# Kernel tuning notes

Measured on AMD Instinct MI355X. Metric: run time of the kernel, lower is better.

Reference implementation:

```python
import jax, jax.numpy as jnp
import numpy as np
from jax import lax

VOCAB, E, H, B, T, NCLS = 50000, 1024, 1024, 1024, 64, 2

def setup_inputs() -> dict:
    key = jax.random.key(0)
    ks = jax.random.split(key, 10)
    s = 0.05
    return {
        "x": jax.random.randint(ks[0], (B, T), 0, VOCAB),
        "emb": jax.random.normal(ks[1], (VOCAB, E), jnp.float32) * s,
        "W_ih": jax.random.normal(ks[2], (4 * H, E), jnp.float32) * s,
        "W_hh": jax.random.normal(ks[3], (4 * H, H), jnp.float32) * s,
        "b_ih": jax.random.normal(ks[4], (4 * H,), jnp.float32) * s,
        "b_hh": jax.random.normal(ks[5], (4 * H,), jnp.float32) * s,
        "W_out": jax.random.normal(ks[6], (NCLS, H), jnp.float32) * s,
        "b_out": jax.random.normal(ks[7], (NCLS,), jnp.float32) * s,
        "h0": jax.random.normal(ks[8], (B, H), jnp.float32),
        "c0": jax.random.normal(ks[9], (B, H), jnp.float32),
    }

def reference(x, emb, W_ih, W_hh, b_ih, b_hh, W_out, b_out, h0, c0):
    # Embedding lookup then transpose to time-major, like x.transpose(1, 0)
    xe = emb[x]                      # [B, T, E]
    xt = jnp.swapaxes(xe, 0, 1)      # [T, B, E]

    def step(carry, xi):
        h, c = carry
        # nn.LSTMCell: gates in (i, f, g, o) order
        gates = xi @ W_ih.T + b_ih + h @ W_hh.T + b_hh  # [B, 4H]
        i, f, g, o = jnp.split(gates, 4, axis=-1)
        c2 = jax.nn.sigmoid(f) * c + jax.nn.sigmoid(i) * jnp.tanh(g)
        h2 = jax.nn.sigmoid(o) * jnp.tanh(c2)
        # Per-step classifier on cell state c (as in the original loop)
        logp = jax.nn.log_softmax(c2 @ W_out.T + b_out, axis=-1)
        return (h2, c2), logp

    (hT, cT), actions_pair = lax.scan(step, (h0, c0), xt)  # actions_pair: [T, B, NCLS]
    out_final = cT @ W_out.T + b_out                       # linear on last cell state
    return actions_pair, out_final
```

## Files before the change

kernel.cpp:

```cpp
#include <hip/hip_runtime.h>

typedef __bf16 bf16x8 __attribute__((ext_vector_type(8)));
typedef float f32x4 __attribute__((ext_vector_type(4)));
typedef unsigned short u16;
typedef unsigned int u32;

#define T_ 64
#define B_ 1024
#define H_ 1024
#define G4_ 4096
#define HB_ (B_ * H_)
#define NBLK_ 512
#define PARTSZ_ (B_ * 2 * 64)

__device__ inline u16 f2bf(float f) {
  u32 u = __float_as_uint(f);
  u32 r = (u + 0x7fffu + ((u >> 16) & 1u)) >> 16;
  return (u16)r;
}

__device__ inline uint2 cvt4(float4 v) {
  uint2 r;
  r.x = (u32)f2bf(v.x) | ((u32)f2bf(v.y) << 16);
  r.y = (u32)f2bf(v.z) | ((u32)f2bf(v.w) << 16);
  return r;
}

__device__ __forceinline__ void gload16(const void* g, void* l) {
  __builtin_amdgcn_global_load_lds(
      (const __attribute__((address_space(1))) unsigned int*)g,
      (__attribute__((address_space(3))) unsigned int*)l, 16, 0, 0);
}

__device__ __forceinline__ void gload16_nt(const void* g, void* l) {
  __builtin_amdgcn_global_load_lds(
      (const __attribute__((address_space(1))) unsigned int*)g,
      (__attribute__((address_space(3))) unsigned int*)l, 16, 0, 2);
}

__device__ __forceinline__ void store_wt16(u16* p, u16 v) {
  asm volatile("global_store_short %0, %1, off sc0 sc1" :: "v"(p), "v"((u32)v) : "memory");
}

__device__ inline float fsig(float x) { return 1.f / (1.f + __expf(-x)); }
__device__ inline float ftanh(float x) {
  float e = __expf(2.f * x);
  return 1.f - 2.f / (e + 1.f);
}

__global__ void prep_kernel(const float* __restrict__ W_ih, const float* __restrict__ W_hh,
                            const float* __restrict__ b_ih, const float* __restrict__ b_hh,
                            const float* __restrict__ h0,
                            u16* __restrict__ WihP, u16* __restrict__ WhhP,
                            float* __restrict__ bcP, u16* __restrict__ h0slot,
                            u32* __restrict__ flags) {
  int bid = blockIdx.x, tid = threadIdx.x;
  if (bid < 4096) {
    int np = bid;
    int gate = (np >> 4) & 3;
    int j = ((np >> 6) << 4) | (np & 15);
    size_t srow = (size_t)(gate * 1024 + j) * 1024;
    int base = tid << 2;
    *(uint2*)(WihP + (size_t)np * 1024 + base) = cvt4(*(const float4*)(W_ih + srow + base));
    *(uint2*)(WhhP + (size_t)np * 1024 + base) = cvt4(*(const float4*)(W_hh + srow + base));
  } else if (bid < 5120) {
    int i = ((bid - 4096) * 256 + tid) << 2;
    *(uint2*)(h0slot + i) = cvt4(*(const float4*)(h0 + i));
  } else if (bid == 5120) {
#pragma unroll
    for (int q = 0; q < 16; ++q) {
      int np = q * 256 + tid;
      int gate = (np >> 4) & 3;
      int j = ((np >> 6) << 4) | (np & 15);
      int srcn = gate * 1024 + j;
      bcP[np] = b_ih[srcn] + b_hh[srcn];
    }
  } else {
    int idx = ((bid - 5121) * 256 + tid) << 2;
    *(uint4*)(flags + idx) = uint4{0u, 0u, 0u, 0u};
  }
}

__global__ void gather_kernel(const int* __restrict__ x, const float* __restrict__ emb,
                              u16* __restrict__ XEall) {
  int b = blockIdx.x, tc = blockIdx.y;
  int row = x[b * T_ + tc];
  int e = threadIdx.x << 2;
  float4 v = *(const float4*)(emb + (size_t)row * H_ + e);
  *(uint2*)(XEall + ((size_t)tc * B_ + b) * H_ + e) = cvt4(v);
}

__global__ void __launch_bounds__(512, 4) xproj_kernel(
    const u16* __restrict__ XEc, const u16* __restrict__ WihP,
    const float* __restrict__ bcP, u16* __restrict__ GXc) {
  __shared__ char smem[49152];
  const int tid = threadIdx.x;
  const int lane = tid & 63;
  const int wave = tid >> 6;
  const int wm = wave >> 1;
  const int wn = wave & 1;
  const int hbid = blockIdx.x;
  const int xcd = hbid & 7;
  const int s10 = hbid >> 3;
  const int mg = s10 >> 6;
  const int rem = s10 & 63;
  const int n0 = (rem >> 1) * 128;
  const int m0 = (xcd * 32 + mg * 2 + (rem & 1)) * 256;

  const u16* srcA[4];
  const u16* srcB[2];
  int betaA[4], betaB[2];
#pragma unroll
  for (int s = 0; s < 4; ++s) {
    int beta = (s * 512 + tid) * 16;
    int row = beta >> 7;
    int colu = (beta & 127) ^ ((row & 7) << 4);
    srcA[s] = XEc + (size_t)(m0 + row) * 1024 + (colu >> 1);
    betaA[s] = beta;
  }
#pragma unroll
  for (int s = 0; s < 2; ++s) {
    int beta = (s * 512 + tid) * 16;
    int row = beta >> 7;
    int colu = (beta & 127) ^ ((row & 7) << 4);
    srcB[s] = WihP + (size_t)(n0 + row) * 1024 + (colu >> 1);
    betaB[s] = 32768 + beta;
  }

  f32x4 acc[4][4] = {};
  const int rsel = lane & 15;
  const int ksel = (lane >> 4) << 4;

  for (int kt = 0; kt < 16; ++kt) {
#pragma unroll
    for (int s = 0; s < 4; ++s) gload16(srcA[s], smem + betaA[s]);
#pragma unroll
    for (int s = 0; s < 2; ++s) gload16(srcB[s], smem + betaB[s]);
#pragma unroll
    for (int s = 0; s < 4; ++s) srcA[s] += 64;
#pragma unroll
    for (int s = 0; s < 2; ++s) srcB[s] += 64;
    __syncthreads();
#pragma unroll
    for (int kk = 0; kk < 2; ++kk) {
      const int colb = kk * 64 + ksel;
      bf16x8 af[4], bfr[4];
#pragma unroll
      for (int mi = 0; mi < 4; ++mi) {
        int row = wm * 64 + mi * 16 + rsel;
        af[mi] = *(const bf16x8*)(smem + row * 128 + (colb ^ ((row & 7) << 4)));
      }
#pragma unroll
      for (int ni = 0; ni < 4; ++ni) {
        int row = wn * 64 + ni * 16 + rsel;
        bfr[ni] = *(const bf16x8*)(smem + 32768 + row * 128 + (colb ^ ((row & 7) << 4)));
      }
#pragma unroll
      for (int mi = 0; mi < 4; ++mi)
#pragma unroll
        for (int ni = 0; ni < 4; ++ni)
          acc[mi][ni] = __builtin_amdgcn_mfma_f32_16x16x32_bf16(af[mi], bfr[ni], acc[mi][ni], 0, 0, 0);
    }
    __syncthreads();
  }

  const int rbase = (lane >> 4) << 2;
  const int cbase = lane & 15;
  float bc[4];
#pragma unroll
  for (int ni = 0; ni < 4; ++ni) bc[ni] = bcP[n0 + wn * 64 + ni * 16 + cbase];
#pragma unroll
  for (int mi = 0; mi < 4; ++mi) {
#pragma unroll
    for (int ni = 0; ni < 4; ++ni) {
      int gc = n0 + wn * 64 + ni * 16 + cbase;
#pragma unroll
      for (int r = 0; r < 4; ++r) {
        int gm = m0 + wm * 64 + mi * 16 + rbase + r;
        GXc[(size_t)gm * G4_ + gc] = f2bf(acc[mi][ni][r] + bc[ni]);
      }
    }
  }
}

__global__ void __launch_bounds__(512, 4) rec_kernel(
    const u16* __restrict__ h0slot, u16* __restrict__ hring,
    const u16* __restrict__ WhhP, const u16* __restrict__ GXall,
    const float* __restrict__ c0, float* __restrict__ partAll,
    const float* __restrict__ Wout, u32* __restrict__ flags) {
  __shared__ char smem[81920];
  const int tid = threadIdx.x;
  const int lane = tid & 63;
  const int qm = tid >> 6;
  const int hbid = blockIdx.x;
  const int L = (hbid & 7) * 64 + (hbid >> 3);
  const int bx = L >> 3;
  const int by = L & 7;
  const int n0 = bx * 64;
  const int m0 = by * 128;

  int offA[2], offGX[2], betaS[2];
  int offB, betaB;
#pragma unroll
  for (int s = 0; s < 2; ++s) {
    int beta = (s * 512 + tid) * 16;
    int row = beta >> 7;
    int colu = (beta & 127) ^ ((row & 7) << 4);
    offA[s] = (m0 + row) * 1024 + (colu >> 1);
    offGX[s] = (m0 + row) * G4_ + n0 + (colu >> 1);
    betaS[s] = beta;
  }
  {
    int beta = tid * 16;
    int row = beta >> 7;
    int colu = (beta & 127) ^ ((row & 7) << 4);
    offB = (n0 + row) * 1024 + (colu >> 1);
    betaB = beta;
  }

  const int rsel = lane & 15;
  const int ksel = (lane >> 4) << 4;
  const int rbase = (lane >> 4) << 2;
  const int cbase = lane & 15;
  const int j = bx * 16 + cbase;
  const float w0 = Wout[j], w1 = Wout[1024 + j];

  float creg[4];
#pragma unroll
  for (int r = 0; r < 4; ++r)
    creg[r] = c0[(size_t)(m0 + qm * 16 + rbase + r) * H_ + j];

#pragma unroll
  for (int s = 0; s < 2; ++s) gload16_nt(GXall + offGX[s], smem + 49152 + betaS[s]);

#pragma unroll 1
  for (int t = 0; t < T_; ++t) {
    gload16(WhhP + offB, smem + 32768 + betaB);

    if (t) {
      if (tid < 64) {
        const u32* fg = flags + (size_t)(t - 1) * NBLK_ + by * 64;
        int guard = 0;
        while (true) {
          u32 v = __hip_atomic_load(fg + tid, __ATOMIC_RELAXED, __HIP_MEMORY_SCOPE_AGENT);
          if (__all(v != 0)) break;
          __builtin_amdgcn_s_sleep(4);
          if (++guard > (1 << 18)) break;
        }
      }
      __syncthreads();
    }

    const u16* hbR = t ? (hring + (size_t)(t - 1) * HB_) : h0slot;
    u16* hbW = hring + (size_t)t * HB_;

#pragma unroll
    for (int s = 0; s < 2; ++s) gload16(hbR + offA[s], smem + betaS[s]);

    f32x4 acc[4] = {};
#pragma unroll
    for (int kt = 0; kt < 16; ++kt) {
      const int cur = kt & 1;
      const int abase = cur * 16384;
      const int bbase = 32768 + cur * 8192;
      if (kt < 15) {
        const int nab = (cur ^ 1) * 16384;
        const int nbb = 32768 + (cur ^ 1) * 8192;
        const int kadv = (kt + 1) * 64;
#pragma unroll
        for (int s = 0; s < 2; ++s) gload16(hbR + offA[s] + kadv, smem + nab + betaS[s]);
        gload16(WhhP + offB + kadv, smem + nbb + betaB);
        asm volatile("s_waitcnt vmcnt(3)" ::: "memory");
      } else {
        asm volatile("s_waitcnt vmcnt(0)" ::: "memory");
      }
      __builtin_amdgcn_s_barrier();
      __builtin_amdgcn_sched_barrier(0);
#pragma unroll
      for (int kk = 0; kk < 2; ++kk) {
        const int colb = kk * 64 + ksel;
        bf16x8 af, bfr[4];
        {
          int row = qm * 16 + rsel;
          af = *(const bf16x8*)(smem + abase + row * 128 + (colb ^ ((row & 7) << 4)));
        }
#pragma unroll
        for (int ni = 0; ni < 4; ++ni) {
          int row = ni * 16 + rsel;
          bfr[ni] = *(const bf16x8*)(smem + bbase + row * 128 + (colb ^ ((row & 7) << 4)));
        }
#pragma unroll
        for (int ni = 0; ni < 4; ++ni)
          acc[ni] = __builtin_amdgcn_mfma_f32_16x16x32_bf16(af, bfr[ni], acc[ni], 0, 0, 0);
      }
      __builtin_amdgcn_s_barrier();
      __builtin_amdgcn_sched_barrier(0);
    }

    const char* lsGX = smem + 49152 + (t & 1) * 16384;
#pragma unroll
    for (int r = 0; r < 4; ++r) {
      int grow = qm * 16 + rbase + r;
      int b = m0 + grow;
      int gxswz = (grow & 7) << 4;
      float gx0 = __uint_as_float(
          (u32)*(const u16*)(lsGX + ((grow << 7) | ((cbase << 1) ^ gxswz))) << 16);
      float gx1 = __uint_as_float(
          (u32)*(const u16*)(lsGX + ((grow << 7) | ((((16 + cbase) << 1)) ^ gxswz))) << 16);
      float gx2 = __uint_as_float(
          (u32)*(const u16*)(lsGX + ((grow << 7) | ((((32 + cbase) << 1)) ^ gxswz))) << 16);
      float gx3 = __uint_as_float(
          (u32)*(const u16*)(lsGX + ((grow << 7) | ((((48 + cbase) << 1)) ^ gxswz))) << 16);
      float gi = acc[0][r] + gx0;
      float gf = acc[1][r] + gx1;
      float gg = acc[2][r] + gx2;
      float go = acc[3][r] + gx3;
      float c2 = fsig(gf) * creg[r] + fsig(gi) * ftanh(gg);
      float h2 = fsig(go) * ftanh(c2);
      creg[r] = c2;
      store_wt16(hbW + (size_t)b * H_ + j, f2bf(h2));
    }

    if (t + 1 < T_) {
      const u16* GXn = GXall + (size_t)(t + 1) * B_ * G4_;
      const int gxb = 49152 + ((t + 1) & 1) * 16384;
#pragma unroll
      for (int s = 0; s < 2; ++s) gload16_nt(GXn + offGX[s], smem + gxb + betaS[s]);
      asm volatile("s_waitcnt vmcnt(2)" ::: "memory");
    } else {
      asm volatile("s_waitcnt vmcnt(0)" ::: "memory");
    }
    __syncthreads();
    if (tid == 0)
      __hip_atomic_store(flags + (size_t)t * NBLK_ + by * 64 + bx, 1u,
                         __ATOMIC_RELAXED, __HIP_MEMORY_SCOPE_AGENT);

    float* partW = partAll + (size_t)t * PARTSZ_;
#pragma unroll
    for (int r = 0; r < 4; ++r) {
      int b = m0 + qm * 16 + rbase + r;
      float p0 = creg[r] * w0, p1 = creg[r] * w1;
#pragma unroll
      for (int off = 1; off < 16; off <<= 1) {
        p0 += __shfl_xor(p0, off);
        p1 += __shfl_xor(p1, off);
      }
      if (cbase == 0) {
        partW[(b << 7) + bx] = p0;
        partW[(b << 7) + 64 + bx] = p1;
      }
    }
  }
}

__global__ void final_kernel(const float* __restrict__ partAll, const float* __restrict__ bout,
                             float* __restrict__ out) {
  int gid = blockIdx.x * 256 + threadIdx.x;
  int t = gid >> 11;
  int r = gid & 2047;
  int b = r >> 1, cls = r & 1;
  const float4* pp = (const float4*)(partAll + (size_t)t * PARTSZ_ + (b << 7) + cls * 64);
  float4 sv = {0.f, 0.f, 0.f, 0.f};
#pragma unroll
  for (int q = 0; q < 16; ++q) {
    float4 v = pp[q];
    sv.x += v.x; sv.y += v.y; sv.z += v.z; sv.w += v.w;
  }
  float l = sv.x + sv.y + sv.z + sv.w + bout[cls];
  float other = __shfl_xor(l, 1);
  float m = fmaxf(l, other);
  float ls = m + __logf(__expf(l - m) + __expf(other - m));
  out[(size_t)t * (B_ * 2) + b * 2 + cls] = l - ls;
  if (t == 63) out[(size_t)T_ * (B_ * 2) + b * 2 + cls] = l;
}

extern "C" void kernel_launch(void* const* d_in, const int* in_sizes, int n_in,
                              void* d_out, int out_size, void* d_ws, size_t ws_size,
                              hipStream_t stream) {
  const int* x      = (const int*)d_in[0];
  const float* emb  = (const float*)d_in[1];
  const float* W_ih = (const float*)d_in[2];
  const float* W_hh = (const float*)d_in[3];
  const float* b_ih = (const float*)d_in[4];
  const float* b_hh = (const float*)d_in[5];
  const float* W_out = (const float*)d_in[6];
  const float* b_out = (const float*)d_in[7];
  const float* h0   = (const float*)d_in[8];
  const float* c0   = (const float*)d_in[9];
  float* out = (float*)d_out;

  char* w = (char*)d_ws;
  u16* WihP = (u16*)w;   w += (size_t)G4_ * H_ * 2;
  u16* WhhP = (u16*)w;   w += (size_t)G4_ * H_ * 2;
  u16* XEall = (u16*)w;  w += (size_t)T_ * HB_ * 2;
  u16* GXall = (u16*)w;  w += (size_t)T_ * B_ * G4_ * 2;
  u16* h0slot = (u16*)w; w += (size_t)HB_ * 2;
  float* bcP = (float*)w;     w += (size_t)G4_ * 4;
  float* partAll = (float*)w; w += (size_t)T_ * PARTSZ_ * 4;
  u32* flags = (u32*)w;       w += (size_t)T_ * NBLK_ * 4;

  prep_kernel<<<5153, 256, 0, stream>>>(W_ih, W_hh, b_ih, b_hh, h0,
                                        WihP, WhhP, bcP, h0slot, flags);
  gather_kernel<<<dim3(B_, T_), 256, 0, stream>>>(x, emb, XEall);
  xproj_kernel<<<8192, 512, 0, stream>>>(XEall, WihP, bcP, GXall);
  rec_kernel<<<NBLK_, 512, 0, stream>>>(h0slot, XEall , WhhP, GXall, c0,
                                        partAll, W_out, flags);
  final_kernel<<<512, 256, 0, stream>>>(partAll, b_out, out);
}
```

Before: 1.606 ms.

## Enlarge recurrent kernel tile to 128x128 with 256 persistent blocks

The recurrent kernel now runs 256 blocks of 256 threads, each owning a 128x128 gate tile instead of 512 blocks with 128x64 tiles. Every wave computes a 4x4 grid of MFMA fragments, which gives more register-level reuse of the A and B fragments and halves the number of blocks polling flags per step. The next step's GX prefetch moves into the last k-iteration so it overlaps with compute. In exchange the kernel uses more LDS and registers per block and has fewer waves to hide latency on each serial timestep.

```diff
diff --git a/kernel.cpp b/kernel.cpp
--- a/kernel.cpp
+++ b/kernel.cpp
@@ -10,7 +10,7 @@
 #define H_ 1024
 #define G4_ 4096
 #define HB_ (B_ * H_)
-#define NBLK_ 512
+#define NBLK_ 256
 #define PARTSZ_ (B_ * 2 * 64)
 
 __device__ inline u16 f2bf(float f) {
@@ -183,70 +183,77 @@
   }
 }
 
-__global__ void __launch_bounds__(512, 4) rec_kernel(
+__global__ void __launch_bounds__(256, 1) rec_kernel(
     const u16* __restrict__ h0slot, u16* __restrict__ hring,
     const u16* __restrict__ WhhP, const u16* __restrict__ GXall,
     const float* __restrict__ c0, float* __restrict__ partAll,
     const float* __restrict__ Wout, u32* __restrict__ flags) {
-  __shared__ char smem[81920];
+  __shared__ char smem[131072];
   const int tid = threadIdx.x;
   const int lane = tid & 63;
-  const int qm = tid >> 6;
+  const int wave = tid >> 6;
+  const int qm = wave >> 1;
+  const int qn = wave & 1;
   const int hbid = blockIdx.x;
-  const int L = (hbid & 7) * 64 + (hbid >> 3);
+  const int L = (hbid & 7) * 32 + (hbid >> 3);
   const int bx = L >> 3;
   const int by = L & 7;
-  const int n0 = bx * 64;
+  const int n0 = bx * 128;
   const int m0 = by * 128;
 
-  int offA[2], offGX[2], betaS[2];
-  int offB, betaB;
-#pragma unroll
-  for (int s = 0; s < 2; ++s) {
-    int beta = (s * 512 + tid) * 16;
+  int offA[4], offB[4], betaS[4];
+  int offGX[8], betaG[8];
+#pragma unroll
+  for (int s = 0; s < 4; ++s) {
+    int beta = (s * 256 + tid) * 16;
     int row = beta >> 7;
     int colu = (beta & 127) ^ ((row & 7) << 4);
     offA[s] = (m0 + row) * 1024 + (colu >> 1);
+    offB[s] = (n0 + row) * 1024 + (colu >> 1);
+    betaS[s] = beta;
+  }
+#pragma unroll
+  for (int s = 0; s < 8; ++s) {
+    int beta = (s * 256 + tid) * 16;
+    int row = beta >> 8;
+    int colu = (beta & 255) ^ ((row & 7) << 4);
     offGX[s] = (m0 + row) * G4_ + n0 + (colu >> 1);
-    betaS[s] = beta;
-  }
-  {
-    int beta = tid * 16;
-    int row = beta >> 7;
-    int colu = (beta & 127) ^ ((row & 7) << 4);
-    offB = (n0 + row) * 1024 + (colu >> 1);
-    betaB = beta;
+    betaG[s] = beta;
   }
 
   const int rsel = lane & 15;
   const int ksel = (lane >> 4) << 4;
   const int rbase = (lane >> 4) << 2;
   const int cbase = lane & 15;
-  const int j = bx * 16 + cbase;
+  const int j = bx * 32 + qn * 16 + cbase;
   const float w0 = Wout[j], w1 = Wout[1024 + j];
 
-  float creg[4];
-#pragma unroll
-  for (int r = 0; r < 4; ++r)
-    creg[r] = c0[(size_t)(m0 + qm * 16 + rbase + r) * H_ + j];
-
-#pragma unroll
-  for (int s = 0; s < 2; ++s) gload16_nt(GXall + offGX[s], smem + 49152 + betaS[s]);
+  float creg[4][4];
+#pragma unroll
+  for (int mi = 0; mi < 4; ++mi)
+#pragma unroll
+    for (int r = 0; r < 4; ++r)
+      creg[mi][r] = c0[(size_t)(m0 + qm * 64 + mi * 16 + rbase + r) * H_ + j];
+
+#pragma unroll
+  for (int s = 0; s < 8; ++s) gload16_nt(GXall + offGX[s], smem + 65536 + betaG[s]);
 
 #pragma unroll 1
   for (int t = 0; t < T_; ++t) {
-    gload16(WhhP + offB, smem + 32768 + betaB);
+#pragma unroll
+    for (int s = 0; s < 4; ++s) gload16(WhhP + offB[s], smem + 32768 + betaS[s]);
 
     if (t) {
-      if (tid < 64) {
-        const u32* fg = flags + (size_t)(t - 1) * NBLK_ + by * 64;
+      if (tid < 32) {
+        const u32* fg = flags + (size_t)(t - 1) * NBLK_ + by * 32;
         int guard = 0;
         while (true) {
           u32 v = __hip_atomic_load(fg + tid, __ATOMIC_RELAXED, __HIP_MEMORY_SCOPE_AGENT);
-          if (__all(v != 0)) break;
+          if (__all(tid >= 32 || v != 0)) break;
           __builtin_amdgcn_s_sleep(4);
           if (++guard > (1 << 18)) break;
         }
+      } else {
       }
       __syncthreads();
     }
@@ -255,99 +262,114 @@
     u16* hbW = hring + (size_t)t * HB_;
 
 #pragma unroll
-    for (int s = 0; s < 2; ++s) gload16(hbR + offA[s], smem + betaS[s]);
-
-    f32x4 acc[4] = {};
+    for (int s = 0; s < 4; ++s) gload16(hbR + offA[s], smem + betaS[s]);
+
+    f32x4 acc[4][4] = {};
 #pragma unroll
     for (int kt = 0; kt < 16; ++kt) {
       const int cur = kt & 1;
       const int abase = cur * 16384;
-      const int bbase = 32768 + cur * 8192;
+      const int bbase = 32768 + cur * 16384;
       if (kt < 15) {
         const int nab = (cur ^ 1) * 16384;
-        const int nbb = 32768 + (cur ^ 1) * 8192;
+        const int nbb = 32768 + (cur ^ 1) * 16384;
         const int kadv = (kt + 1) * 64;
 #pragma unroll
-        for (int s = 0; s < 2; ++s) gload16(hbR + offA[s] + kadv, smem + nab + betaS[s]);
-        gload16(WhhP + offB + kadv, smem + nbb + betaB);
-        asm volatile("s_waitcnt vmcnt(3)" ::: "memory");
+        for (int s = 0; s < 4; ++s) gload16(hbR + offA[s] + kadv, smem + nab + betaS[s]);
+#pragma unroll
+        for (int s = 0; s < 4; ++s) gload16(WhhP + offB[s] + kadv, smem + nbb + betaS[s]);
+        asm volatile("s_waitcnt vmcnt(8)" ::: "memory");
       } else {
-        asm volatile("s_waitcnt vmcnt(0)" ::: "memory");
+        if (t + 1 < T_) {
+          const u16* GXn = GXall + (size_t)(t + 1) * B_ * G4_;
+          const int gxb = 65536 + ((t + 1) & 1) * 32768;
+#pragma unroll
+          for (int s = 0; s < 8; ++s) gload16_nt(GXn + offGX[s], smem + gxb + betaG[s]);
+          asm volatile("s_waitcnt vmcnt(8)" ::: "memory");
+        } else {
+          asm volatile("s_waitcnt vmcnt(0)" ::: "memory");
+        }
       }
       __builtin_amdgcn_s_barrier();
       __builtin_amdgcn_sched_barrier(0);
 #pragma unroll
       for (int kk = 0; kk < 2; ++kk) {
         const int colb = kk * 64 + ksel;
-        bf16x8 af, bfr[4];
-        {
-          int row = qm * 16 + rsel;
-          af = *(const bf16x8*)(smem + abase + row * 128 + (colb ^ ((row & 7) << 4)));
+        bf16x8 af[4], bfr[4];
+#pragma unroll
+        for (int mi = 0; mi < 4; ++mi) {
+          int row = qm * 64 + mi * 16 + rsel;
+          af[mi] = *(const bf16x8*)(smem + abase + row * 128 + (colb ^ ((row & 7) << 4)));
         }
 #pragma unroll
         for (int ni = 0; ni < 4; ++ni) {
-          int row = ni * 16 + rsel;
+          int row = qn * 64 + ni * 16 + rsel;
           bfr[ni] = *(const bf16x8*)(smem + bbase + row * 128 + (colb ^ ((row & 7) << 4)));
         }
 #pragma unroll
-        for (int ni = 0; ni < 4; ++ni)
-          acc[ni] = __builtin_amdgcn_mfma_f32_16x16x32_bf16(af, bfr[ni], acc[ni], 0, 0, 0);
+        for (int mi = 0; mi < 4; ++mi)
+#pragma unroll
+          for (int ni = 0; ni < 4; ++ni)
+            acc[mi][ni] = __builtin_amdgcn_mfma_f32_16x16x32_bf16(af[mi], bfr[ni], acc[mi][ni], 0, 0, 0);
       }
       __builtin_amdgcn_s_barrier();
       __builtin_amdgcn_sched_barrier(0);
     }
 
-    const char* lsGX = smem + 49152 + (t & 1) * 16384;
-#pragma unroll
-    for (int r = 0; r < 4; ++r) {
-      int grow = qm * 16 + rbase + r;
-      int b = m0 + grow;
-      int gxswz = (grow & 7) << 4;
-      float gx0 = __uint_as_float(
-          (u32)*(const u16*)(lsGX + ((grow << 7) | ((cbase << 1) ^ gxswz))) << 16);
-      float gx1 = __uint_as_float(
-          (u32)*(const u16*)(lsGX + ((grow << 7) | ((((16 + cbase) << 1)) ^ gxswz))) << 16);
-      float gx2 = __uint_as_float(
-          (u32)*(const u16*)(lsGX + ((grow << 7) | ((((32 + cbase) << 1)) ^ gxswz))) << 16);
-      float gx3 = __uint_as_float(
-          (u32)*(const u16*)(lsGX + ((grow << 7) | ((((48 + cbase) << 1)) ^ gxswz))) << 16);
-      float gi = acc[0][r] + gx0;
-      float gf = acc[1][r] + gx1;
-      float gg = acc[2][r] + gx2;
-      float go = acc[3][r] + gx3;
-      float c2 = fsig(gf) * creg[r] + fsig(gi) * ftanh(gg);
-      float h2 = fsig(go) * ftanh(c2);
-      creg[r] = c2;
-      store_wt16(hbW + (size_t)b * H_ + j, f2bf(h2));
+    const char* lsGX = smem + 65536 + (t & 1) * 32768;
+#pragma unroll
+    for (int mi = 0; mi < 4; ++mi) {
+#pragma unroll
+      for (int r = 0; r < 4; ++r) {
+        int grow = qm * 64 + mi * 16 + rbase + r;
+        int b = m0 + grow;
+        int gxswz = (grow & 7) << 4;
+        const char* gxrow = lsGX + (grow << 8);
+        float gx0 = __uint_as_float(
+            (u32)*(const u16*)(gxrow + ((((qn * 64 + cbase) << 1)) ^ gxswz)) << 16);
+        float gx1 = __uint_as_float(
+            (u32)*(const u16*)(gxrow + ((((qn * 64 + 16 + cbase) << 1)) ^ gxswz)) << 16);
+        float gx2 = __uint_as_float(
+            (u32)*(const u16*)(gxrow + ((((qn * 64 + 32 + cbase) << 1)) ^ gxswz)) << 16);
+        float gx3 = __uint_as_float(
+            (u32)*(const u16*)(gxrow + ((((qn * 64 + 48 + cbase) << 1)) ^ gxswz)) << 16);
+        float gi = acc[mi][0][r] + gx0;
+        float gf = acc[mi][1][r] + gx1;
+        float gg = acc[mi][2][r] + gx2;
+        float go = acc[mi][3][r] + gx3;
+        float c2 = fsig(gf) * creg[mi][r] + fsig(gi) * ftanh(gg);
+        float h2 = fsig(go) * ftanh(c2);
+        creg[mi][r] = c2;
+        store_wt16(hbW + (size_t)b * H_ + j, f2bf(h2));
+      }
     }
 
     if (t + 1 < T_) {
-      const u16* GXn = GXall + (size_t)(t + 1) * B_ * G4_;
-      const int gxb = 49152 + ((t + 1) & 1) * 16384;
-#pragma unroll
-      for (int s = 0; s < 2; ++s) gload16_nt(GXn + offGX[s], smem + gxb + betaS[s]);
-      asm volatile("s_waitcnt vmcnt(2)" ::: "memory");
+      asm volatile("s_waitcnt vmcnt(8)" ::: "memory");
     } else {
       asm volatile("s_waitcnt vmcnt(0)" ::: "memory");
     }
     __syncthreads();
     if (tid == 0)
-      __hip_atomic_store(flags + (size_t)t * NBLK_ + by * 64 + bx, 1u,
+      __hip_atomic_store(flags + (size_t)t * NBLK_ + by * 32 + bx, 1u,
                          __ATOMIC_RELAXED, __HIP_MEMORY_SCOPE_AGENT);
 
     float* partW = partAll + (size_t)t * PARTSZ_;
 #pragma unroll
-    for (int r = 0; r < 4; ++r) {
-      int b = m0 + qm * 16 + rbase + r;
-      float p0 = creg[r] * w0, p1 = creg[r] * w1;
-#pragma unroll
-      for (int off = 1; off < 16; off <<= 1) {
-        p0 += __shfl_xor(p0, off);
-        p1 += __shfl_xor(p1, off);
-      }
-      if (cbase == 0) {
-        partW[(b << 7) + bx] = p0;
-        partW[(b << 7) + 64 + bx] = p1;
+    for (int mi = 0; mi < 4; ++mi) {
+#pragma unroll
+      for (int r = 0; r < 4; ++r) {
+        int b = m0 + qm * 64 + mi * 16 + rbase + r;
+        float p0 = creg[mi][r] * w0, p1 = creg[mi][r] * w1;
+#pragma unroll
+        for (int off = 1; off < 16; off <<= 1) {
+          p0 += __shfl_xor(p0, off);
+          p1 += __shfl_xor(p1, off);
+        }
+        if (cbase == 0) {
+          partW[(b << 7) + (bx << 1) + qn] = p0;
+          partW[(b << 7) + 64 + (bx << 1) + qn] = p1;
+        }
       }
     }
   }
@@ -399,11 +421,11 @@
   float* partAll = (float*)w; w += (size_t)T_ * PARTSZ_ * 4;
   u32* flags = (u32*)w;       w += (size_t)T_ * NBLK_ * 4;
 
-  prep_kernel<<<5153, 256, 0, stream>>>(W_ih, W_hh, b_ih, b_hh, h0,
+  prep_kernel<<<5137, 256, 0, stream>>>(W_ih, W_hh, b_ih, b_hh, h0,
                                         WihP, WhhP, bcP, h0slot, flags);
   gather_kernel<<<dim3(B_, T_), 256, 0, stream>>>(x, emb, XEall);
   xproj_kernel<<<8192, 512, 0, stream>>>(XEall, WihP, bcP, GXall);
-  rec_kernel<<<NBLK_, 512, 0, stream>>>(h0slot, XEall , WhhP, GXall, c0,
+  rec_kernel<<<NBLK_, 256, 0, stream>>>(h0slot, XEall , WhhP, GXall, c0,
                                         partAll, W_out, flags);
   final_kernel<<<512, 256, 0, stream>>>(partAll, b_out, out);
 }
```

Result: slower. 1.721 ms (+7.2%).

## Store input-gate projections in per-thread fragment layout and triple-buffer recurrent K-loop

Applied to the files above, without the earlier changes.

The xproj kernel now writes its bf16 outputs permuted so each recurrent-kernel thread reads its 16 gate pre-activations with two contiguous 16-byte global loads, replacing the LDS staging of GX tiles and the scalar LDS reads. The recurrent kernel's K-loop goes from double to triple buffering with a prefetch distance of two, using the LDS freed by dropping the GX buffers. This is meant to cut per-step LDS traffic and hide more global-load latency, but the GX loads are now issued at the top of each step, and the xproj stores become a scattered layout.

```diff
diff --git a/kernel.cpp b/kernel.cpp
--- a/kernel.cpp
+++ b/kernel.cpp
@@ -19,6 +19,8 @@
   return (u16)r;
 }
 
+__device__ inline float bf2f(u16 v) { return __uint_as_float((u32)v << 16); }
+
 __device__ inline uint2 cvt4(float4 v) {
   uint2 r;
   r.x = (u32)f2bf(v.x) | ((u32)f2bf(v.y) << 16);
@@ -30,12 +32,6 @@
   __builtin_amdgcn_global_load_lds(
       (const __attribute__((address_space(1))) unsigned int*)g,
       (__attribute__((address_space(3))) unsigned int*)l, 16, 0, 0);
-}
-
-__device__ __forceinline__ void gload16_nt(const void* g, void* l) {
-  __builtin_amdgcn_global_load_lds(
-      (const __attribute__((address_space(1))) unsigned int*)g,
-      (__attribute__((address_space(3))) unsigned int*)l, 16, 0, 2);
 }
 
 __device__ __forceinline__ void store_wt16(u16* p, u16 v) {
@@ -92,7 +88,7 @@
 
 __global__ void __launch_bounds__(512, 4) xproj_kernel(
     const u16* __restrict__ XEc, const u16* __restrict__ WihP,
-    const float* __restrict__ bcP, u16* __restrict__ GXc) {
+    const float* __restrict__ bcP, u16* __restrict__ GX2) {
   __shared__ char smem[49152];
   const int tid = threadIdx.x;
   const int lane = tid & 63;
@@ -169,26 +165,33 @@
   float bc[4];
 #pragma unroll
   for (int ni = 0; ni < 4; ++ni) bc[ni] = bcP[n0 + wn * 64 + ni * 16 + cbase];
+  const int tstep = m0 >> 10;
+  const int bxp = (n0 >> 6) + wn;
+  const int brow0 = (m0 & 1023) + wm * 64;
 #pragma unroll
   for (int mi = 0; mi < 4; ++mi) {
-#pragma unroll
-    for (int ni = 0; ni < 4; ++ni) {
-      int gc = n0 + wn * 64 + ni * 16 + cbase;
-#pragma unroll
-      for (int r = 0; r < 4; ++r) {
-        int gm = m0 + wm * 64 + mi * 16 + rbase + r;
-        GXc[(size_t)gm * G4_ + gc] = f2bf(acc[mi][ni][r] + bc[ni]);
-      }
-    }
+    int brow = brow0 + mi * 16;
+    int byp = brow >> 7;
+    int qmp = (brow >> 4) & 7;
+    int tidp = qmp * 64 + (rbase << 2) + cbase;
+    size_t gb = (((size_t)tstep * NBLK_ + bxp * 8 + byp) * 512 + tidp) * 16;
+    u16 vals[16];
+#pragma unroll
+    for (int ni = 0; ni < 4; ++ni)
+#pragma unroll
+      for (int r = 0; r < 4; ++r)
+        vals[ni * 4 + r] = f2bf(acc[mi][ni][r] + bc[ni]);
+    *(uint4*)(GX2 + gb) = *(const uint4*)vals;
+    *(uint4*)(GX2 + gb + 8) = *(const uint4*)(vals + 8);
   }
 }
 
 __global__ void __launch_bounds__(512, 4) rec_kernel(
     const u16* __restrict__ h0slot, u16* __restrict__ hring,
-    const u16* __restrict__ WhhP, const u16* __restrict__ GXall,
+    const u16* __restrict__ WhhP, const u16* __restrict__ GX2,
     const float* __restrict__ c0, float* __restrict__ partAll,
     const float* __restrict__ Wout, u32* __restrict__ flags) {
-  __shared__ char smem[81920];
+  __shared__ char smem[73728];
   const int tid = threadIdx.x;
   const int lane = tid & 63;
   const int qm = tid >> 6;
@@ -199,7 +202,7 @@
   const int n0 = bx * 64;
   const int m0 = by * 128;
 
-  int offA[2], offGX[2], betaS[2];
+  int offA[2], betaS[2];
   int offB, betaB;
 #pragma unroll
   for (int s = 0; s < 2; ++s) {
@@ -207,7 +210,6 @@
     int row = beta >> 7;
     int colu = (beta & 127) ^ ((row & 7) << 4);
     offA[s] = (m0 + row) * 1024 + (colu >> 1);
-    offGX[s] = (m0 + row) * G4_ + n0 + (colu >> 1);
     betaS[s] = beta;
   }
   {
@@ -225,17 +227,20 @@
   const int j = bx * 16 + cbase;
   const float w0 = Wout[j], w1 = Wout[1024 + j];
 
+  const u16* gptr = GX2 + ((size_t)(bx * 8 + by) * 512 + tid) * 16;
+
   float creg[4];
 #pragma unroll
   for (int r = 0; r < 4; ++r)
     creg[r] = c0[(size_t)(m0 + qm * 16 + rbase + r) * H_ + j];
 
-#pragma unroll
-  for (int s = 0; s < 2; ++s) gload16_nt(GXall + offGX[s], smem + 49152 + betaS[s]);
-
 #pragma unroll 1
   for (int t = 0; t < T_; ++t) {
-    gload16(WhhP + offB, smem + 32768 + betaB);
+    const u16* gp = gptr + (size_t)t * (NBLK_ * 512 * 16);
+    uint4 gxa = *(const uint4*)gp;
+    uint4 gxb = *(const uint4*)(gp + 8);
+
+    gload16(WhhP + offB, smem + 49152 + betaB);
 
     if (t) {
       if (tid < 64) {
@@ -256,20 +261,25 @@
 
 #pragma unroll
     for (int s = 0; s < 2; ++s) gload16(hbR + offA[s], smem + betaS[s]);
+#pragma unroll
+    for (int s = 0; s < 2; ++s) gload16(hbR + offA[s] + 64, smem + 16384 + betaS[s]);
+    gload16(WhhP + offB + 64, smem + 49152 + 8192 + betaB);
 
     f32x4 acc[4] = {};
 #pragma unroll
     for (int kt = 0; kt < 16; ++kt) {
-      const int cur = kt & 1;
+      const int cur = kt % 3;
       const int abase = cur * 16384;
-      const int bbase = 32768 + cur * 8192;
-      if (kt < 15) {
-        const int nab = (cur ^ 1) * 16384;
-        const int nbb = 32768 + (cur ^ 1) * 8192;
-        const int kadv = (kt + 1) * 64;
-#pragma unroll
-        for (int s = 0; s < 2; ++s) gload16(hbR + offA[s] + kadv, smem + nab + betaS[s]);
-        gload16(WhhP + offB + kadv, smem + nbb + betaB);
+      const int bbase = 49152 + cur * 8192;
+      if (kt < 14) {
+        const int nxt = (kt + 2) % 3;
+        const int kadv = (kt + 2) * 64;
+#pragma unroll
+        for (int s = 0; s < 2; ++s)
+          gload16(hbR + offA[s] + kadv, smem + nxt * 16384 + betaS[s]);
+        gload16(WhhP + offB + kadv, smem + 49152 + nxt * 8192 + betaB);
+        asm volatile("s_waitcnt vmcnt(6)" ::: "memory");
+      } else if (kt == 14) {
         asm volatile("s_waitcnt vmcnt(3)" ::: "memory");
       } else {
         asm volatile("s_waitcnt vmcnt(0)" ::: "memory");
@@ -297,39 +307,23 @@
       __builtin_amdgcn_sched_barrier(0);
     }
 
-    const char* lsGX = smem + 49152 + (t & 1) * 16384;
+    u16 gxs[16];
+    *(uint4*)gxs = gxa;
+    *(uint4*)(gxs + 8) = gxb;
 #pragma unroll
     for (int r = 0; r < 4; ++r) {
-      int grow = qm * 16 + rbase + r;
-      int b = m0 + grow;
-      int gxswz = (grow & 7) << 4;
-      float gx0 = __uint_as_float(
-          (u32)*(const u16*)(lsGX + ((grow << 7) | ((cbase << 1) ^ gxswz))) << 16);
-      float gx1 = __uint_as_float(
-          (u32)*(const u16*)(lsGX + ((grow << 7) | ((((16 + cbase) << 1)) ^ gxswz))) << 16);
-      float gx2 = __uint_as_float(
-          (u32)*(const u16*)(lsGX + ((grow << 7) | ((((32 + cbase) << 1)) ^ gxswz))) << 16);
-      float gx3 = __uint_as_float(
-          (u32)*(const u16*)(lsGX + ((grow << 7) | ((((48 + cbase) << 1)) ^ gxswz))) << 16);
-      float gi = acc[0][r] + gx0;
-      float gf = acc[1][r] + gx1;
-      float gg = acc[2][r] + gx2;
-      float go = acc[3][r] + gx3;
+      int b = m0 + qm * 16 + rbase + r;
+      float gi = acc[0][r] + bf2f(gxs[r]);
+      float gf = acc[1][r] + bf2f(gxs[4 + r]);
+      float gg = acc[2][r] + bf2f(gxs[8 + r]);
+      float go = acc[3][r] + bf2f(gxs[12 + r]);
       float c2 = fsig(gf) * creg[r] + fsig(gi) * ftanh(gg);
       float h2 = fsig(go) * ftanh(c2);
       creg[r] = c2;
       store_wt16(hbW + (size_t)b * H_ + j, f2bf(h2));
     }
 
-    if (t + 1 < T_) {
-      const u16* GXn = GXall + (size_t)(t + 1) * B_ * G4_;
-      const int gxb = 49152 + ((t + 1) & 1) * 16384;
-#pragma unroll
-      for (int s = 0; s < 2; ++s) gload16_nt(GXn + offGX[s], smem + gxb + betaS[s]);
-      asm volatile("s_waitcnt vmcnt(2)" ::: "memory");
-    } else {
-      asm volatile("s_waitcnt vmcnt(0)" ::: "memory");
-    }
+    asm volatile("s_waitcnt vmcnt(0)" ::: "memory");
     __syncthreads();
     if (tid == 0)
       __hip_atomic_store(flags + (size_t)t * NBLK_ + by * 64 + bx, 1u,
@@ -393,7 +387,7 @@
   u16* WihP = (u16*)w;   w += (size_t)G4_ * H_ * 2;
   u16* WhhP = (u16*)w;   w += (size_t)G4_ * H_ * 2;
   u16* XEall = (u16*)w;  w += (size_t)T_ * HB_ * 2;
-  u16* GXall = (u16*)w;  w += (size_t)T_ * B_ * G4_ * 2;
+  u16* GX2  = (u16*)w;   w += (size_t)T_ * NBLK_ * 512 * 16 * 2;
   u16* h0slot = (u16*)w; w += (size_t)HB_ * 2;
   float* bcP = (float*)w;     w += (size_t)G4_ * 4;
   float* partAll = (float*)w; w += (size_t)T_ * PARTSZ_ * 4;
@@ -402,8 +396,8 @@
   prep_kernel<<<5153, 256, 0, stream>>>(W_ih, W_hh, b_ih, b_hh, h0,
                                         WihP, WhhP, bcP, h0slot, flags);
   gather_kernel<<<dim3(B_, T_), 256, 0, stream>>>(x, emb, XEall);
-  xproj_kernel<<<8192, 512, 0, stream>>>(XEall, WihP, bcP, GXall);
-  rec_kernel<<<NBLK_, 512, 0, stream>>>(h0slot, XEall , WhhP, GXall, c0,
+  xproj_kernel<<<8192, 512, 0, stream>>>(XEall, WihP, bcP, GX2);
+  rec_kernel<<<NBLK_, 512, 0, stream>>>(h0slot, XEall , WhhP, GX2, c0,
                                         partAll, W_out, flags);
   final_kernel<<<512, 256, 0, stream>>>(partAll, b_out, out);
 }
```

Measured after the change: 1.601 ms. About the same (-0.3%).
